# Performance work log

Measured on AMD Instinct MI355X. Metric: run time of the kernel, lower is better.

## Reference

```python
import jax, jax.numpy as jnp
import numpy as np
from jax import lax

# --- model constants (match init_kwargs) ---
B = 4096
T, N_FEAT = 100, 81
KH = 7                 # cnn_kernel_height
T_MOD = T - KH + 1     # 94
M = 100                # cnn_hidden_size
P = 128                # decoder hidden size
SKIP = 10
SH = 32                # skip_hidden_size
PT = T_MOD // SKIP     # 9


def setup_inputs() -> dict:
    key = jax.random.key(0)
    ks = jax.random.split(key, 18)
    s = 0.05
    def rn(k, shape, scale=s):
        return jax.random.normal(k, shape, dtype=jnp.float32) * scale
    return {
        "enc_data": jax.random.normal(ks[0], (B, T, N_FEAT), dtype=jnp.float32),
        # Conv2d(1 -> M, kernel=(KH, N_FEAT))
        "conv_w": rn(ks[1], (M, 1, KH, N_FEAT)),
        "conv_b": rn(ks[2], (M,)),
        # TemporalAttention: W_d: Linear(2P->M, no bias), U_d: Linear(M->M, no bias), v_d: Linear(M->1, no bias)
        "Wd": rn(ks[3], (M, 2 * P)),
        "Ud": rn(ks[4], (M, M)),
        "vd": rn(ks[5], (1, M)),
        # LSTM(input=M, hidden=P), PyTorch gate order i,f,g,o
        "lstm_wih": rn(ks[6], (4 * P, M)),
        "lstm_whh": rn(ks[7], (4 * P, P)),
        "lstm_bih": rn(ks[8], (4 * P,)),
        "lstm_bhh": rn(ks[9], (4 * P,)),
        # GRU(input=M, hidden=SH), PyTorch gate order r,z,n
        "gru_wih": rn(ks[10], (3 * SH, M)),
        "gru_whh": rn(ks[11], (3 * SH, SH)),
        "gru_bih": rn(ks[12], (3 * SH,)),
        "gru_bhh": rn(ks[13], (3 * SH,)),
        # output head: Linear(M+P+SKIP*SH -> P), ReLU, (Dropout=eval identity), Linear(P -> 1)
        "out1_w": rn(ks[14], (P, M + P + SKIP * SH)),
        "out1_b": rn(ks[15], (P,)),
        "out2_w": rn(ks[16], (1, P)),
        "out2_b": rn(ks[17], (1,)),
    }


def reference(enc_data, conv_w, conv_b, Wd, Ud, vd,
              lstm_wih, lstm_whh, lstm_bih, lstm_bhh,
              gru_wih, gru_whh, gru_bih, gru_bhh,
              out1_w, out1_b, out2_w, out2_b):
    b = enc_data.shape[0]

    # --- CNN encoder: Conv2d valid over full feature width -> [B, T_MOD, M] ---
    x = enc_data[:, None]  # [B,1,T,n]
    h = lax.conv_general_dilated(x, conv_w, window_strides=(1, 1), padding='VALID',
                                 dimension_numbers=('NCHW', 'OIHW', 'NCHW'))  # [B,M,T_MOD,1]
    H = jax.nn.relu(h + conv_b[None, :, None, None])[..., 0].transpose(0, 2, 1)  # [B,T_MOD,M]

    # precompute U_d(H) once (same math; U_d applied to H is step-invariant)
    HU = jnp.einsum('btm,km->btk', H, Ud)  # [B,T_MOD,M]

    def dec_step(carry, _):
        d, s = carry  # each [B,P]
        q = jnp.concatenate([d, s], axis=1)                       # [B,2P]
        e = jnp.tanh((q @ Wd.T)[:, None, :] + HU)                 # [B,T_MOD,M]
        scores = jnp.einsum('btm,m->bt', e, vd[0])                # [B,T_MOD]
        beta = jax.nn.softmax(scores, axis=1)                     # softmax over time
        c = jnp.einsum('bt,btm->bm', beta, H)                     # context [B,M]
        gates = c @ lstm_wih.T + lstm_bih + d @ lstm_whh.T + lstm_bhh
        i_g, f_g, g_g, o_g = jnp.split(gates, 4, axis=1)
        s_new = jax.nn.sigmoid(f_g) * s + jax.nn.sigmoid(i_g) * jnp.tanh(g_g)
        d_new = jax.nn.sigmoid(o_g) * jnp.tanh(s_new)
        return (d_new, s_new), (beta, c)

    d0 = jnp.zeros((b, P), dtype=enc_data.dtype)
    s0 = jnp.zeros((b, P), dtype=enc_data.dtype)
    (d_T, _), (betas, cs) = lax.scan(dec_step, (d0, s0), None, length=T_MOD)
    c_last = cs[-1]                                               # [B,M]
    dec_out = jnp.concatenate([d_T, c_last], axis=1)              # [B, P+M]

    # --- skip GRU over strided conv features ---
    Hs = H[:, -PT * SKIP:, :]                                     # [B, PT*SKIP, M]
    Hs = (Hs.transpose(0, 2, 1)                                   # [B, M, PT*SKIP]
            .reshape(b, M, PT, SKIP)
            .transpose(2, 0, 3, 1)                                # [PT, B, SKIP, M]
            .reshape(PT, b * SKIP, M))

    def gru_step(hprev, xt):
        gi = xt @ gru_wih.T + gru_bih
        gh = hprev @ gru_whh.T + gru_bhh
        ir, iz, inn = jnp.split(gi, 3, axis=1)
        hr, hz, hn = jnp.split(gh, 3, axis=1)
        r = jax.nn.sigmoid(ir + hr)
        z = jax.nn.sigmoid(iz + hz)
        nn_ = jnp.tanh(inn + r * hn)
        hnew = (1.0 - z) * nn_ + z * hprev
        return hnew, None

    h0 = jnp.zeros((b * SKIP, SH), dtype=enc_data.dtype)
    h_skip, _ = lax.scan(gru_step, h0, Hs)                        # [B*SKIP, SH]
    h_skip = h_skip.reshape(b, SKIP * SH)                         # matches torch view

    feat = jnp.concatenate([dec_out, h_skip], axis=1)             # [B, P+M+SKIP*SH]
    out = jax.nn.relu(feat @ out1_w.T + out1_b) @ out2_w.T + out2_b  # [B,1]
    return out[:, 0]
```

## Files before the change

kernel.cpp:

```cpp
#include <hip/hip_runtime.h>

typedef unsigned int u32;
typedef unsigned short u16;
typedef _Float16 half2_t __attribute__((ext_vector_type(2)));

#define TM 94
#define NB 2
#define DEC_NT 512

__device__ __forceinline__ float bf2f(u16 v){ return __builtin_bit_cast(float, ((u32)v)<<16); }
__device__ __forceinline__ float bflo(u32 v){ return __builtin_bit_cast(float, v<<16); }
__device__ __forceinline__ float bfhi(u32 v){ return __builtin_bit_cast(float, v & 0xffff0000u); }
__device__ __forceinline__ u32 f2bf_bits(float f){ u32 u=__builtin_bit_cast(u32,f); return (u + 0x7fffu + ((u>>16)&1u))>>16; }
__device__ __forceinline__ u32 packbf2(float a, float b){ return f2bf_bits(a) | (f2bf_bits(b)<<16); }
__device__ __forceinline__ u32 packh2(float a, float b){ half2_t h; h.x=(_Float16)a; h.y=(_Float16)b; return __builtin_bit_cast(u32,h); }
__device__ __forceinline__ float fdot2(u32 a, u32 b, float c){
  return __builtin_amdgcn_fdot2(__builtin_bit_cast(half2_t,a), __builtin_bit_cast(half2_t,b), c, false);
}
__device__ __forceinline__ float fast_rcp(float x){ return __builtin_amdgcn_rcpf(x); }
__device__ __forceinline__ float sigmoid_f(float x){ return fast_rcp(1.f + __expf(-x)); }
__device__ __forceinline__ float tanh_f(float x){ float e=__expf(2.f*x); return 1.f - 2.f*fast_rcp(e+1.f); }

__global__ __launch_bounds__(256)
void prep_kernel(const float* __restrict__ wih, const float* __restrict__ whh,
                 const float* __restrict__ Wd,
                 uint4* __restrict__ WgT, uint4* __restrict__ WdT2)
{
  int idx = blockIdx.x*256 + threadIdx.x;
  if (idx < 16384){
    int t = idx & 1023;
    int j = idx >> 10;
    int h = t >> 9, g = t & 511;
    u32 r[4];
    #pragma unroll
    for (int s=0;s<4;s++){
      int u = 4*j + s;
      u32 v = 0u;
      if (h==0){ if (u < 50) v = packh2(wih[g*100+2*u], wih[g*100+2*u+1]); }
      else     { if (u < 64) v = packh2(whh[g*128+2*u], whh[g*128+2*u+1]); }
      r[s]=v;
    }
    WgT[idx] = make_uint4(r[0],r[1],r[2],r[3]);
  } else {
    int idx2 = idx - 16384;
    int t = idx2 & 511;
    int i = idx2 >> 9;
    int mw = t >> 2, part = t & 3;
    u32 r[4] = {0u,0u,0u,0u};
    if (mw < 100){
      int ii = (i + 2*part) & 7;
      const float* wd = Wd + mw*256 + 2*(part*32 + ii*4);
      #pragma unroll
      for (int k=0;k<4;k++) r[k] = packh2(wd[2*k], wd[2*k+1]);
    }
    WdT2[idx2] = make_uint4(r[0],r[1],r[2],r[3]);
  }
}

__global__ __launch_bounds__(128)
void conv_kernel(const float* __restrict__ enc, const float* __restrict__ cw,
                 const float* __restrict__ cb, u16* __restrict__ Hb)
{
  __shared__ float sE[8100];
  const int tid = threadIdx.x;
  const int b = blockIdx.y;
  const int chunk = blockIdx.x;
  const float* ep = enc + (size_t)b*8100;
  for (int i=tid;i<8100;i+=128) sE[i]=ep[i];
  __syncthreads();
  if (tid >= TM) return;
  const int t = tid;
  const int mo = chunk*10;
  const float* wb = cw + mo*567;
  float acc[10];
  #pragma unroll
  for (int k=0;k<10;k++) acc[k]=cb[mo+k];
  const float* e = sE + t*81;
  #pragma unroll 3
  for (int j=0;j<567;j++){
    float ev = e[j];
    #pragma unroll
    for (int k=0;k<10;k++) acc[k] += ev*wb[k*567+j];
  }
  u32* out = (u32*)Hb + ((size_t)b*9400 + t*100 + mo)/2;
  #pragma unroll
  for (int k=0;k<5;k++) out[k] = packbf2(fmaxf(acc[2*k],0.f), fmaxf(acc[2*k+1],0.f));
}

#define OFF_SHU 37600
#define OFF_SQ  75200
#define OFF_SZ  76224
#define OFF_SVD 77248
#define OFF_AB  77648
#define DEC_LDS 79696

__global__ __launch_bounds__(DEC_NT) __attribute__((amdgpu_waves_per_eu(2, 4)))
void decoder_kernel(const u16* __restrict__ Hb, const float* __restrict__ Ud,
                    const float* __restrict__ vd,
                    const uint4* __restrict__ WgT, const uint4* __restrict__ WdT2,
                    const float* __restrict__ bih, const float* __restrict__ bhh,
                    float* __restrict__ dT, float* __restrict__ cLast)
{
  extern __shared__ char smem[];
  u16*      sH   = (u16*)smem;
  u16*      sHU  = (u16*)(smem + OFF_SHU);
  u32*      sq32 = (u32*)(smem + OFF_SQ);
  _Float16* sq16 = (_Float16*)(smem + OFF_SQ);
  u32*      sz32 = (u32*)(smem + OFF_SZ);
  _Float16* sz16 = (_Float16*)(smem + OFF_SZ);
  float*    svd  = (float*)(smem + OFF_SVD);
  float*    sa   = (float*)(smem + OFF_AB);
  float*    sbeta= (float*)(smem + OFF_AB + 800);
  _Float16* sg16 = (_Float16*)(smem + OFF_AB);

  const int tid = threadIdx.x;
  const int b0 = blockIdx.x * NB;

  {
    const uint4* src = (const uint4*)(Hb + (size_t)b0*9400);
    uint4* dst = (uint4*)sH;
    for (int i=tid;i<2350;i+=DEC_NT) dst[i]=src[i];
  }
  if (tid < 100) svd[tid] = vd[tid];
  for (int i=tid;i<NB*128;i+=DEC_NT){ sq32[i]=0u; sz32[i]=0u; }
  __syncthreads();

  for (int idx=tid; idx<4700; idx+=DEC_NT){
    int kq = idx/188;
    int r  = idx - kq*188;
    int bi = r/94;
    int t  = r - 94*bi;
    const u32* hrow = (const u32*)sH + bi*4700 + t*50;
    const float* ud0 = Ud + (kq*4+0)*100;
    const float* ud1 = Ud + (kq*4+1)*100;
    const float* ud2 = Ud + (kq*4+2)*100;
    const float* ud3 = Ud + (kq*4+3)*100;
    float c0=0.f,c1=0.f,c2=0.f,c3=0.f;
    #pragma unroll 5
    for (int mq=0; mq<25; mq++){
      uint2 hp = *(const uint2*)(hrow + mq*2);
      float h0=bflo(hp.x), h1=bfhi(hp.x), h2=bflo(hp.y), h3=bfhi(hp.y);
      float4 u0 = *(const float4*)(ud0 + mq*4);
      float4 u1 = *(const float4*)(ud1 + mq*4);
      float4 u2 = *(const float4*)(ud2 + mq*4);
      float4 u3 = *(const float4*)(ud3 + mq*4);
      c0 += h0*u0.x + h1*u0.y + h2*u0.z + h3*u0.w;
      c1 += h0*u1.x + h1*u1.y + h2*u1.z + h3*u1.w;
      c2 += h0*u2.x + h1*u2.y + h2*u2.z + h3*u2.w;
      c3 += h0*u3.x + h1*u3.y + h2*u3.z + h3*u3.w;
    }
    u32* dst = (u32*)sHU + bi*4700 + t*50 + kq*2;
    dst[0] = packbf2(c0,c1);
    dst[1] = packbf2(c2,c3);
  }
  __syncthreads();

  const int mw = tid>>2, part = tid&3;
  uint4 wv[8];
  if (mw < 100){
    #pragma unroll
    for (int i=0;i<8;i++) wv[i] = WdT2[i*512 + tid];
  }
  const float biasg = bih[tid] + bhh[tid];
  const uint4* wp0 = WgT + tid;
  const uint4* wp1 = WgT + 512 + tid;

  float s_reg = 0.f;

  #pragma unroll 1
  for (int step=0; step<TM; step++){
    if (mw < 100){
      #pragma unroll 1
      for (int bi=0;bi<NB;bi++){
        const u32* qb = sq32 + bi*128 + part*32;
        float a0=0.f, a1=0.f;
        #pragma unroll
        for (int i=0;i<8;i++){
          int ii = (i+2*part)&7;
          uint4 qv = *(const uint4*)(qb + ii*4);
          a0 = fdot2(wv[i].x, qv.x, a0);
          a1 = fdot2(wv[i].y, qv.y, a1);
          a0 = fdot2(wv[i].z, qv.z, a0);
          a1 = fdot2(wv[i].w, qv.w, a1);
        }
        float acc = a0+a1;
        acc += __shfl_xor(acc,1);
        acc += __shfl_xor(acc,2);
        if (part==0) sa[bi*100+mw]=acc;
      }
    }
    __syncthreads();
    if (tid < NB*188){
      int row = tid>>1, th = tid&1;
      int bi = row/94;
      int t  = row - 94*bi;
      const uint4* hu4 = (const uint4*)((const u32*)sHU + bi*4700 + t*50 + th*24);
      const float4* ap = (const float4*)(sa + bi*100) + th*12;
      const float4* vp = (const float4*)svd + th*12;
      float acc=0.f;
      #pragma unroll
      for (int c=0;c<6;c++){
        uint4 h4 = hu4[c];
        float4 a0 = ap[2*c], a1 = ap[2*c+1];
        float4 v0 = vp[2*c], v1 = vp[2*c+1];
        acc += v0.x*tanh_f(a0.x + bflo(h4.x));
        acc += v0.y*tanh_f(a0.y + bfhi(h4.x));
        acc += v0.z*tanh_f(a0.z + bflo(h4.y));
        acc += v0.w*tanh_f(a0.w + bfhi(h4.y));
        acc += v1.x*tanh_f(a1.x + bflo(h4.z));
        acc += v1.y*tanh_f(a1.y + bfhi(h4.z));
        acc += v1.z*tanh_f(a1.z + bflo(h4.w));
        acc += v1.w*tanh_f(a1.w + bfhi(h4.w));
      }
      if (th){
        uint2 ht = *(const uint2*)((const u32*)hu4 + 24);
        float4 a = ap[12]; float4 v = vp[12];
        acc += v.x*tanh_f(a.x + bflo(ht.x));
        acc += v.y*tanh_f(a.y + bfhi(ht.x));
        acc += v.z*tanh_f(a.z + bflo(ht.y));
        acc += v.w*tanh_f(a.w + bfhi(ht.y));
      }
      acc += __shfl_xor(acc,1);
      if (!th) sbeta[bi*96+t]=acc;
    }
    __syncthreads();
    if (tid < 64*NB){
      int bi = tid>>6, lane = tid&63;
      float s0 = sbeta[bi*96+lane];
      float s1 = (lane<30)? sbeta[bi*96+64+lane] : -1e30f;
      float mx = fmaxf(s0,s1);
      #pragma unroll
      for (int o=32;o>=1;o>>=1) mx = fmaxf(mx, __shfl_xor(mx,o));
      float e0 = __expf(s0-mx);
      float e1 = (lane<30)? __expf(s1-mx) : 0.f;
      float sm = e0+e1;
      #pragma unroll
      for (int o=32;o>=1;o>>=1) sm += __shfl_xor(sm,o);
      float rs = fast_rcp(sm);
      sbeta[bi*96+lane] = e0*rs;
      if (lane<30) sbeta[bi*96+64+lane] = e1*rs;
    }
    __syncthreads();
    if (tid < NB*200){
      int bi = tid/200;
      int r  = tid - 200*bi;
      int mp = r>>2, th = r&3;
      int tstart = (th<2) ? th*24 : 48+(th-2)*23;
      const float* bp = sbeta + bi*96 + tstart;
      const u32* hp = (const u32*)sH + bi*4700 + tstart*50 + mp;
      float a0=0.f, a1=0.f;
      #pragma unroll
      for (int i=0;i<23;i++){
        float be = bp[i];
        u32 h = hp[i*50];
        a0 += be*bflo(h); a1 += be*bfhi(h);
      }
      if (th<2){
        float be = bp[23]; u32 h = hp[23*50];
        a0 += be*bflo(h); a1 += be*bfhi(h);
      }
      a0 += __shfl_xor(a0,1); a1 += __shfl_xor(a1,1);
      a0 += __shfl_xor(a0,2); a1 += __shfl_xor(a1,2);
      if (th==0){
        sz32[bi*128+mp] = packh2(a0,a1);
        if (step==TM-1){
          cLast[(size_t)(b0+bi)*100 + 2*mp]   = a0;
          cLast[(size_t)(b0+bi)*100 + 2*mp+1] = a1;
        }
      }
    }
    __syncthreads();
    {
      float acc0 = biasg, acc1 = biasg;
      const u32* zc0 = sz32;
      const u32* zc1 = sz32 + 128;
      #pragma unroll 1
      for (int jb=0; jb<16; jb+=4){
        uint4 w[4], v[4];
        #pragma unroll
        for (int k=0;k<4;k++) w[k] = wp0[(jb+k)*1024];
        #pragma unroll
        for (int k=0;k<4;k++) v[k] = wp1[(jb+k)*1024];
        #pragma unroll
        for (int k=0;k<4;k++){
          int j = jb+k;
          uint4 zA0 = *(const uint4*)(zc0 + 4*j);
          uint4 zA1 = *(const uint4*)(zc1 + 4*j);
          acc0 = fdot2(w[k].x, zA0.x, acc0); acc0 = fdot2(w[k].y, zA0.y, acc0);
          acc0 = fdot2(w[k].z, zA0.z, acc0); acc0 = fdot2(w[k].w, zA0.w, acc0);
          acc1 = fdot2(w[k].x, zA1.x, acc1); acc1 = fdot2(w[k].y, zA1.y, acc1);
          acc1 = fdot2(w[k].z, zA1.z, acc1); acc1 = fdot2(w[k].w, zA1.w, acc1);
          uint4 zB0 = *(const uint4*)(zc0 + 64 + 4*j);
          uint4 zB1 = *(const uint4*)(zc1 + 64 + 4*j);
          acc0 = fdot2(v[k].x, zB0.x, acc0); acc0 = fdot2(v[k].y, zB0.y, acc0);
          acc0 = fdot2(v[k].z, zB0.z, acc0); acc0 = fdot2(v[k].w, zB0.w, acc0);
          acc1 = fdot2(v[k].x, zB1.x, acc1); acc1 = fdot2(v[k].y, zB1.y, acc1);
          acc1 = fdot2(v[k].z, zB1.z, acc1); acc1 = fdot2(v[k].w, zB1.w, acc1);
        }
      }
      sg16[      tid] = (_Float16)acc0;
      sg16[512 + tid] = (_Float16)acc1;
    }
    __syncthreads();
    if (tid < 128*NB){
      int bi = tid>>7, p = tid&127;
      float ig = (float)sg16[bi*512+p];
      float fg = (float)sg16[bi*512+128+p];
      float gg_= (float)sg16[bi*512+256+p];
      float og = (float)sg16[bi*512+384+p];
      float sn = sigmoid_f(fg)*s_reg + sigmoid_f(ig)*tanh_f(gg_);
      float dn = sigmoid_f(og)*tanh_f(sn);
      s_reg = sn;
      sq16[bi*256+p]      = (_Float16)dn;
      sq16[bi*256+128+p]  = (_Float16)sn;
      sz16[bi*256+128+p]  = (_Float16)dn;
      if (step==TM-1) dT[(size_t)(b0+bi)*128+p]=dn;
    }
    __syncthreads();
  }
}

__global__ __launch_bounds__(256)
void gru_kernel(const u16* __restrict__ Hb, const float* __restrict__ wih,
                const float* __restrict__ whh, const float* __restrict__ bihp,
                const float* __restrict__ bhhp, float* __restrict__ hskip)
{
  __shared__ float sWih[96][101];
  __shared__ float sWhh[96][33];
  __shared__ float sxt[8][100];
  __shared__ float sh[8][33];
  const int tid = threadIdx.x;
  for (int i=tid;i<9600;i+=256){ sWih[i/100][i%100]=wih[i]; }
  for (int i=tid;i<3072;i+=256){ sWhh[i>>5][i&31]=whh[i]; }
  const int r = tid>>5, j = tid&31;
  const int rowg = blockIdx.x*8 + r;
  const int b = rowg/10, sk = rowg - b*10;
  const float b_r = bihp[j], b_z = bihp[32+j], b_n = bihp[64+j];
  const float hb_r = bhhp[j], hb_z = bhhp[32+j], hb_n = bhhp[64+j];
  sh[r][j]=0.f;
  float h = 0.f;
  __syncthreads();
  for (int pt=0; pt<9; pt++){
    for (int i=tid;i<800;i+=256){
      int rr=i/100, m=i-rr*100;
      int rg = blockIdx.x*8+rr; int bb=rg/10, ss=rg-bb*10;
      sxt[rr][m] = bf2f(Hb[(size_t)bb*9400 + (size_t)(4+pt*10+ss)*100 + m]);
    }
    __syncthreads();
    float gi_r=b_r, gi_z=b_z, gi_n=b_n, gh_r=hb_r, gh_z=hb_z, gh_n=hb_n;
    #pragma unroll 4
    for (int m=0;m<100;m++){
      float x = sxt[r][m];
      gi_r += sWih[j][m]*x; gi_z += sWih[32+j][m]*x; gi_n += sWih[64+j][m]*x;
    }
    #pragma unroll
    for (int k=0;k<32;k++){
      float hp = sh[r][k];
      gh_r += sWhh[j][k]*hp; gh_z += sWhh[32+j][k]*hp; gh_n += sWhh[64+j][k]*hp;
    }
    float rg_ = sigmoid_f(gi_r+gh_r);
    float z  = sigmoid_f(gi_z+gh_z);
    float n  = tanh_f(gi_n + rg_*gh_n);
    h = (1.f-z)*n + z*h;
    __syncthreads();
    sh[r][j]=h;
    __syncthreads();
  }
  hskip[(size_t)b*320 + sk*32 + j] = h;
}

#define OUT_NB 32
#define OUT_LDS ((OUT_NB*552 + 8*552)*4)

__global__ __launch_bounds__(256)
void out_kernel(const float* __restrict__ dT, const float* __restrict__ cLast,
                const float* __restrict__ hskip, const float* __restrict__ w1,
                const float* __restrict__ b1, const float* __restrict__ w2,
                const float* __restrict__ b2, float* __restrict__ outp)
{
  extern __shared__ float osm[];
  float* sf = osm;
  float* sw = osm + OUT_NB*552;
  const int tid = threadIdx.x;
  const int b0 = blockIdx.x*OUT_NB;
  for (int i=tid;i<OUT_NB*548;i+=256){
    int bl = i/548, k = i - 548*bl; int b = b0+bl;
    float v;
    if (k<128) v = dT[(size_t)b*128+k];
    else if (k<228) v = cLast[(size_t)b*100+(k-128)];
    else v = hskip[(size_t)b*320+(k-228)];
    sf[bl*552+k]=v;
  }
  const int bl = tid>>3, j = tid&7;
  float outv = 0.f;
  for (int jt=0; jt<128; jt+=8){
    __syncthreads();
    for (int i=tid;i<8*548;i+=256){
      int rr=i/548, c=i-548*rr;
      sw[rr*552+c] = w1[(size_t)jt*548 + i];
    }
    __syncthreads();
    float acc = b1[jt+j];
    const float* fr = sf + bl*552;
    const float* wr = sw + j*552;
    #pragma unroll 4
    for (int k=0;k<548;k++) acc += fr[k]*wr[k];
    outv += fmaxf(acc,0.f)*w2[jt+j];
  }
  outv += __shfl_xor(outv,1);
  outv += __shfl_xor(outv,2);
  outv += __shfl_xor(outv,4);
  if (j==0) outp[b0+bl] = outv + b2[0];
}

extern "C" void kernel_launch(void* const* d_in, const int* in_sizes, int n_in,
                              void* d_out, int out_size, void* d_ws, size_t ws_size,
                              hipStream_t stream)
{
  const float* enc      = (const float*)d_in[0];
  const float* conv_w   = (const float*)d_in[1];
  const float* conv_b   = (const float*)d_in[2];
  const float* Wd       = (const float*)d_in[3];
  const float* Ud       = (const float*)d_in[4];
  const float* vd       = (const float*)d_in[5];
  const float* lstm_wih = (const float*)d_in[6];
  const float* lstm_whh = (const float*)d_in[7];
  const float* lstm_bih = (const float*)d_in[8];
  const float* lstm_bhh = (const float*)d_in[9];
  const float* gru_wih  = (const float*)d_in[10];
  const float* gru_whh  = (const float*)d_in[11];
  const float* gru_bih  = (const float*)d_in[12];
  const float* gru_bhh  = (const float*)d_in[13];
  const float* out1_w   = (const float*)d_in[14];
  const float* out1_b   = (const float*)d_in[15];
  const float* out2_w   = (const float*)d_in[16];
  const float* out2_b   = (const float*)d_in[17];

  char* ws = (char*)d_ws;
  u16*   Hb    = (u16*)ws;
  float* dT    = (float*)(ws + 77004800);
  float* cLast = (float*)(ws + 79101952);
  float* hskip = (float*)(ws + 80740352);
  uint4* WgT   = (uint4*)(ws + 80740352);
  uint4* WdT2  = (uint4*)(ws + 81002496);

  prep_kernel<<<80, 256, 0, stream>>>(lstm_wih, lstm_whh, Wd, WgT, WdT2);

  conv_kernel<<<dim3(10,4096,1), 128, 0, stream>>>(enc, conv_w, conv_b, Hb);

  (void)hipFuncSetAttribute((const void*)decoder_kernel,
                            hipFuncAttributeMaxDynamicSharedMemorySize, DEC_LDS);
  decoder_kernel<<<4096/NB, DEC_NT, DEC_LDS, stream>>>(Hb, Ud, vd, WgT, WdT2,
                                                       lstm_bih, lstm_bhh,
                                                       dT, cLast);

  gru_kernel<<<5120, 256, 0, stream>>>(Hb, gru_wih, gru_whh, gru_bih, gru_bhh, hskip);

  (void)hipFuncSetAttribute((const void*)out_kernel,
                            hipFuncAttributeMaxDynamicSharedMemorySize, OUT_LDS);
  out_kernel<<<4096/OUT_NB, 256, OUT_LDS, stream>>>(dT, cLast, hskip, out1_w, out1_b,
                                                    out2_w, out2_b, (float*)d_out);
}
```

Measured before the change: 7.351 ms.

## Move attention U_d projection to global scratch and halve decoder LDS footprint

The decoder kernel now keeps the precomputed H·U_d projection in a per-block global scratch buffer (padded rows) instead of LDS. The d/s/z vectors are packed into one compact shared region, with the weight layout in prep_kernel reordered to match, so the attention and gate dot products skip the zero-padded words. LDS per block drops to about half, which should let more blocks sit on each CU. The grid is fixed at 1024 persistent blocks that each process two batch pairs in sequence. The cost is per-step global/L2 reads of the projection instead of LDS reads, and fewer blocks in the grid.

Result: slower. 8.167 ms (+11.1%).

```diff
diff --git a/kernel.cpp b/kernel.cpp
--- a/kernel.cpp
+++ b/kernel.cpp
@@ -7,6 +7,7 @@
 #define TM 94
 #define NB 2
 #define DEC_NT 512
+#define DEC_GRID 1024
 
 __device__ __forceinline__ float bf2f(u16 v){ return __builtin_bit_cast(float, ((u32)v)<<16); }
 __device__ __forceinline__ float bflo(u32 v){ return __builtin_bit_cast(float, v<<16); }
@@ -24,7 +25,7 @@
 __global__ __launch_bounds__(256)
 void prep_kernel(const float* __restrict__ wih, const float* __restrict__ whh,
                  const float* __restrict__ Wd,
-                 uint4* __restrict__ WgT, uint4* __restrict__ WdT2)
+                 uint4* __restrict__ WgT, uint4* __restrict__ WdT3)
 {
   int idx = blockIdx.x*256 + threadIdx.x;
   if (idx < 16384){
@@ -48,12 +49,12 @@
     int mw = t >> 2, part = t & 3;
     u32 r[4] = {0u,0u,0u,0u};
     if (mw < 100){
-      int ii = (i + 2*part) & 7;
-      const float* wd = Wd + mw*256 + 2*(part*32 + ii*4);
+      int bu = (i<4) ? (part*16 + 4*i) : (64 + part*16 + 4*(i-4));
+      const float* wd = Wd + mw*256 + 2*bu;
       #pragma unroll
       for (int k=0;k<4;k++) r[k] = packh2(wd[2*k], wd[2*k+1]);
     }
-    WdT2[idx2] = make_uint4(r[0],r[1],r[2],r[3]);
+    WdT3[idx2] = make_uint4(r[0],r[1],r[2],r[3]);
   }
 }
 
@@ -87,236 +88,257 @@
   for (int k=0;k<5;k++) out[k] = packbf2(fmaxf(acc[2*k],0.f), fmaxf(acc[2*k+1],0.f));
 }
 
-#define OFF_SHU 37600
-#define OFF_SQ  75200
-#define OFF_SZ  76224
-#define OFF_SVD 77248
-#define OFF_AB  77648
-#define DEC_LDS 79696
+#define OFF_SZQ   37600
+#define OFF_STAIL 38624
+#define OFF_UNI   38752
+#define DEC_LDS   40800
 
 __global__ __launch_bounds__(DEC_NT) __attribute__((amdgpu_waves_per_eu(2, 4)))
 void decoder_kernel(const u16* __restrict__ Hb, const float* __restrict__ Ud,
                     const float* __restrict__ vd,
-                    const uint4* __restrict__ WgT, const uint4* __restrict__ WdT2,
+                    const uint4* __restrict__ WgT, const uint4* __restrict__ WdT3,
                     const float* __restrict__ bih, const float* __restrict__ bhh,
-                    float* __restrict__ dT, float* __restrict__ cLast)
+                    u32* __restrict__ HUscr, float* __restrict__ dT,
+                    float* __restrict__ cLast)
 {
   extern __shared__ char smem[];
   u16*      sH   = (u16*)smem;
-  u16*      sHU  = (u16*)(smem + OFF_SHU);
-  u32*      sq32 = (u32*)(smem + OFF_SQ);
-  _Float16* sq16 = (_Float16*)(smem + OFF_SQ);
-  u32*      sz32 = (u32*)(smem + OFF_SZ);
-  _Float16* sz16 = (_Float16*)(smem + OFF_SZ);
-  float*    svd  = (float*)(smem + OFF_SVD);
-  float*    sa   = (float*)(smem + OFF_AB);
-  float*    sbeta= (float*)(smem + OFF_AB + 800);
-  _Float16* sg16 = (_Float16*)(smem + OFF_AB);
+  float*    sa   = (float*)(smem + OFF_UNI);
+  float*    sbeta= (float*)(smem + OFF_UNI + 800);
+  _Float16* sg16 = (_Float16*)(smem + OFF_UNI);
 
   const int tid = threadIdx.x;
-  const int b0 = blockIdx.x * NB;
-
-  {
-    const uint4* src = (const uint4*)(Hb + (size_t)b0*9400);
-    uint4* dst = (uint4*)sH;
-    for (int i=tid;i<2350;i+=DEC_NT) dst[i]=src[i];
-  }
-  if (tid < 100) svd[tid] = vd[tid];
-  for (int i=tid;i<NB*128;i+=DEC_NT){ sq32[i]=0u; sz32[i]=0u; }
-  __syncthreads();
-
-  for (int idx=tid; idx<4700; idx+=DEC_NT){
-    int kq = idx/188;
-    int r  = idx - kq*188;
-    int bi = r/94;
-    int t  = r - 94*bi;
-    const u32* hrow = (const u32*)sH + bi*4700 + t*50;
-    const float* ud0 = Ud + (kq*4+0)*100;
-    const float* ud1 = Ud + (kq*4+1)*100;
-    const float* ud2 = Ud + (kq*4+2)*100;
-    const float* ud3 = Ud + (kq*4+3)*100;
-    float c0=0.f,c1=0.f,c2=0.f,c3=0.f;
-    #pragma unroll 5
-    for (int mq=0; mq<25; mq++){
-      uint2 hp = *(const uint2*)(hrow + mq*2);
-      float h0=bflo(hp.x), h1=bfhi(hp.x), h2=bflo(hp.y), h3=bfhi(hp.y);
-      float4 u0 = *(const float4*)(ud0 + mq*4);
-      float4 u1 = *(const float4*)(ud1 + mq*4);
-      float4 u2 = *(const float4*)(ud2 + mq*4);
-      float4 u3 = *(const float4*)(ud3 + mq*4);
-      c0 += h0*u0.x + h1*u0.y + h2*u0.z + h3*u0.w;
-      c1 += h0*u1.x + h1*u1.y + h2*u1.z + h3*u1.w;
-      c2 += h0*u2.x + h1*u2.y + h2*u2.z + h3*u2.w;
-      c3 += h0*u3.x + h1*u3.y + h2*u3.z + h3*u3.w;
-    }
-    u32* dst = (u32*)sHU + bi*4700 + t*50 + kq*2;
-    dst[0] = packbf2(c0,c1);
-    dst[1] = packbf2(c2,c3);
-  }
-  __syncthreads();
-
   const int mw = tid>>2, part = tid&3;
+
   uint4 wv[8];
   if (mw < 100){
     #pragma unroll
-    for (int i=0;i<8;i++) wv[i] = WdT2[i*512 + tid];
+    for (int i=0;i<8;i++) wv[i] = WdT3[i*512 + tid];
   }
   const float biasg = bih[tid] + bhh[tid];
   const uint4* wp0 = WgT + tid;
   const uint4* wp1 = WgT + 512 + tid;
-
-  float s_reg = 0.f;
+  u32* hub = HUscr + (size_t)blockIdx.x * 9776;
 
   #pragma unroll 1
-  for (int step=0; step<TM; step++){
-    if (mw < 100){
-      #pragma unroll 1
-      for (int bi=0;bi<NB;bi++){
-        const u32* qb = sq32 + bi*128 + part*32;
+  for (int pr=0; pr<2; ++pr){
+    const int pair = blockIdx.x + pr*DEC_GRID;
+    const int b0 = pair*NB;
+
+    {
+      const uint4* src = (const uint4*)(Hb + (size_t)b0*9400);
+      uint4* dst = (uint4*)sH;
+      for (int i=tid;i<2350;i+=DEC_NT) dst[i]=src[i];
+      for (int i=tid;i<288;i+=DEC_NT) ((u32*)(smem+OFF_SZQ))[i]=0u;
+    }
+    __syncthreads();
+    for (int idx=tid; idx<4700; idx+=DEC_NT){
+      int kq = idx/188;
+      int r  = idx - kq*188;
+      int bi = r/94;
+      int t  = r - 94*bi;
+      const u32* hrow = (const u32*)sH + bi*4700 + t*50;
+      const float* ud0 = Ud + (kq*4+0)*100;
+      const float* ud1 = Ud + (kq*4+1)*100;
+      const float* ud2 = Ud + (kq*4+2)*100;
+      const float* ud3 = Ud + (kq*4+3)*100;
+      float c0=0.f,c1=0.f,c2=0.f,c3=0.f;
+      #pragma unroll 5
+      for (int mq=0; mq<25; mq++){
+        uint2 hp = *(const uint2*)(hrow + mq*2);
+        float h0=bflo(hp.x), h1=bfhi(hp.x), h2=bflo(hp.y), h3=bfhi(hp.y);
+        float4 u0 = *(const float4*)(ud0 + mq*4);
+        float4 u1 = *(const float4*)(ud1 + mq*4);
+        float4 u2 = *(const float4*)(ud2 + mq*4);
+        float4 u3 = *(const float4*)(ud3 + mq*4);
+        c0 += h0*u0.x + h1*u0.y + h2*u0.z + h3*u0.w;
+        c1 += h0*u1.x + h1*u1.y + h2*u1.z + h3*u1.w;
+        c2 += h0*u2.x + h1*u2.y + h2*u2.z + h3*u2.w;
+        c3 += h0*u3.x + h1*u3.y + h2*u3.z + h3*u3.w;
+      }
+      u32* dst = hub + bi*4888 + t*52 + kq*2;
+      dst[0] = packbf2(c0,c1);
+      dst[1] = packbf2(c2,c3);
+    }
+    float s_reg = 0.f;
+    __syncthreads();
+
+    #pragma unroll 1
+    for (int step=0; step<TM; step++){
+      if (mw < 100){
+        #pragma unroll 1
+        for (int bi=0;bi<NB;bi++){
+          const char* zb = smem + OFF_SZQ + bi*512;
+          const uint4* qd = (const uint4*)(zb + 208) + part*4;
+          const uint4* qs = (part<3) ? ((const uint4*)zb + part*4)
+                                     : (const uint4*)(smem + OFF_STAIL + bi*64);
+          float a0=0.f, a1=0.f;
+          #pragma unroll
+          for (int i=0;i<4;i++){
+            uint4 qv = qd[i];
+            a0 = fdot2(wv[i].x, qv.x, a0);
+            a1 = fdot2(wv[i].y, qv.y, a1);
+            a0 = fdot2(wv[i].z, qv.z, a0);
+            a1 = fdot2(wv[i].w, qv.w, a1);
+          }
+          #pragma unroll
+          for (int i=0;i<4;i++){
+            uint4 qv = qs[i];
+            a0 = fdot2(wv[4+i].x, qv.x, a0);
+            a1 = fdot2(wv[4+i].y, qv.y, a1);
+            a0 = fdot2(wv[4+i].z, qv.z, a0);
+            a1 = fdot2(wv[4+i].w, qv.w, a1);
+          }
+          float acc = a0+a1;
+          acc += __shfl_xor(acc,1);
+          acc += __shfl_xor(acc,2);
+          if (part==0) sa[bi*100+mw]=acc;
+        }
+      }
+      __syncthreads();
+      if (tid < 376){
+        int row = tid>>1, th = tid&1;
+        int bi = row/94;
+        int t  = row - 94*bi;
+        const uint4* hu4 = (const uint4*)(hub + bi*4888 + t*52) + th*6;
+        const float4* ap = (const float4*)(sa + bi*100) + th*12;
+        const float4* vp = (const float4*)vd + th*12;
+        float acc=0.f;
+        #pragma unroll
+        for (int c=0;c<6;c++){
+          uint4 h4 = hu4[c];
+          float4 a0 = ap[2*c], a1 = ap[2*c+1];
+          float4 v0 = vp[2*c], v1 = vp[2*c+1];
+          acc += v0.x*tanh_f(a0.x + bflo(h4.x));
+          acc += v0.y*tanh_f(a0.y + bfhi(h4.x));
+          acc += v0.z*tanh_f(a0.z + bflo(h4.y));
+          acc += v0.w*tanh_f(a0.w + bfhi(h4.y));
+          acc += v1.x*tanh_f(a1.x + bflo(h4.z));
+          acc += v1.y*tanh_f(a1.y + bfhi(h4.z));
+          acc += v1.z*tanh_f(a1.z + bflo(h4.w));
+          acc += v1.w*tanh_f(a1.w + bfhi(h4.w));
+        }
+        if (th){
+          uint2 ht = *(const uint2*)((const u32*)hu4 + 24);
+          float4 a = ap[12]; float4 v = vp[12];
+          acc += v.x*tanh_f(a.x + bflo(ht.x));
+          acc += v.y*tanh_f(a.y + bfhi(ht.x));
+          acc += v.z*tanh_f(a.z + bflo(ht.y));
+          acc += v.w*tanh_f(a.w + bfhi(ht.y));
+        }
+        acc += __shfl_xor(acc,1);
+        if (!th) sbeta[bi*96+t]=acc;
+      }
+      __syncthreads();
+      if (tid < 64*NB){
+        int bi = tid>>6, lane = tid&63;
+        float s0 = sbeta[bi*96+lane];
+        float s1 = (lane<30)? sbeta[bi*96+64+lane] : -1e30f;
+        float mx = fmaxf(s0,s1);
+        #pragma unroll
+        for (int o=32;o>=1;o>>=1) mx = fmaxf(mx, __shfl_xor(mx,o));
+        float e0 = __expf(s0-mx);
+        float e1 = (lane<30)? __expf(s1-mx) : 0.f;
+        float sm = e0+e1;
+        #pragma unroll
+        for (int o=32;o>=1;o>>=1) sm += __shfl_xor(sm,o);
+        float rs = fast_rcp(sm);
+        sbeta[bi*96+lane] = e0*rs;
+        if (lane<30) sbeta[bi*96+64+lane] = e1*rs;
+      }
+      __syncthreads();
+      if (tid < NB*200){
+        int bi = tid/200;
+        int r  = tid - 200*bi;
+        int mp = r>>2, th = r&3;
+        int tstart = (th<2) ? th*24 : 48+(th-2)*23;
+        const float* bp = sbeta + bi*96 + tstart;
+        const u32* hp = (const u32*)sH + bi*4700 + tstart*50 + mp;
         float a0=0.f, a1=0.f;
         #pragma unroll
-        for (int i=0;i<8;i++){
-          int ii = (i+2*part)&7;
-          uint4 qv = *(const uint4*)(qb + ii*4);
-          a0 = fdot2(wv[i].x, qv.x, a0);
-          a1 = fdot2(wv[i].y, qv.y, a1);
-          a0 = fdot2(wv[i].z, qv.z, a0);
-          a1 = fdot2(wv[i].w, qv.w, a1);
-        }
-        float acc = a0+a1;
-        acc += __shfl_xor(acc,1);
-        acc += __shfl_xor(acc,2);
-        if (part==0) sa[bi*100+mw]=acc;
-      }
-    }
-    __syncthreads();
-    if (tid < NB*188){
-      int row = tid>>1, th = tid&1;
-      int bi = row/94;
-      int t  = row - 94*bi;
-      const uint4* hu4 = (const uint4*)((const u32*)sHU + bi*4700 + t*50 + th*24);
-      const float4* ap = (const float4*)(sa + bi*100) + th*12;
-      const float4* vp = (const float4*)svd + th*12;
-      float acc=0.f;
-      #pragma unroll
-      for (int c=0;c<6;c++){
-        uint4 h4 = hu4[c];
-        float4 a0 = ap[2*c], a1 = ap[2*c+1];
-        float4 v0 = vp[2*c], v1 = vp[2*c+1];
-        acc += v0.x*tanh_f(a0.x + bflo(h4.x));
-        acc += v0.y*tanh_f(a0.y + bfhi(h4.x));
-        acc += v0.z*tanh_f(a0.z + bflo(h4.y));
-        acc += v0.w*tanh_f(a0.w + bfhi(h4.y));
-        acc += v1.x*tanh_f(a1.x + bflo(h4.z));
-        acc += v1.y*tanh_f(a1.y + bfhi(h4.z));
-        acc += v1.z*tanh_f(a1.z + bflo(h4.w));
-        acc += v1.w*tanh_f(a1.w + bfhi(h4.w));
-      }
-      if (th){
-        uint2 ht = *(const uint2*)((const u32*)hu4 + 24);
-        float4 a = ap[12]; float4 v = vp[12];
-        acc += v.x*tanh_f(a.x + bflo(ht.x));
-        acc += v.y*tanh_f(a.y + bfhi(ht.x));
-        acc += v.z*tanh_f(a.z + bflo(ht.y));
-        acc += v.w*tanh_f(a.w + bfhi(ht.y));
-      }
-      acc += __shfl_xor(acc,1);
-      if (!th) sbeta[bi*96+t]=acc;
-    }
-    __syncthreads();
-    if (tid < 64*NB){
-      int bi = tid>>6, lane = tid&63;
-      float s0 = sbeta[bi*96+lane];
-      float s1 = (lane<30)? sbeta[bi*96+64+lane] : -1e30f;
-      float mx = fmaxf(s0,s1);
-      #pragma unroll
-      for (int o=32;o>=1;o>>=1) mx = fmaxf(mx, __shfl_xor(mx,o));
-      float e0 = __expf(s0-mx);
-      float e1 = (lane<30)? __expf(s1-mx) : 0.f;
-      float sm = e0+e1;
-      #pragma unroll
-      for (int o=32;o>=1;o>>=1) sm += __shfl_xor(sm,o);
-      float rs = fast_rcp(sm);
-      sbeta[bi*96+lane] = e0*rs;
-      if (lane<30) sbeta[bi*96+64+lane] = e1*rs;
-    }
-    __syncthreads();
-    if (tid < NB*200){
-      int bi = tid/200;
-      int r  = tid - 200*bi;
-      int mp = r>>2, th = r&3;
-      int tstart = (th<2) ? th*24 : 48+(th-2)*23;
-      const float* bp = sbeta + bi*96 + tstart;
-      const u32* hp = (const u32*)sH + bi*4700 + tstart*50 + mp;
-      float a0=0.f, a1=0.f;
-      #pragma unroll
-      for (int i=0;i<23;i++){
-        float be = bp[i];
-        u32 h = hp[i*50];
-        a0 += be*bflo(h); a1 += be*bfhi(h);
-      }
-      if (th<2){
-        float be = bp[23]; u32 h = hp[23*50];
-        a0 += be*bflo(h); a1 += be*bfhi(h);
-      }
-      a0 += __shfl_xor(a0,1); a1 += __shfl_xor(a1,1);
-      a0 += __shfl_xor(a0,2); a1 += __shfl_xor(a1,2);
-      if (th==0){
-        sz32[bi*128+mp] = packh2(a0,a1);
-        if (step==TM-1){
-          cLast[(size_t)(b0+bi)*100 + 2*mp]   = a0;
-          cLast[(size_t)(b0+bi)*100 + 2*mp+1] = a1;
-        }
-      }
-    }
-    __syncthreads();
-    {
-      float acc0 = biasg, acc1 = biasg;
-      const u32* zc0 = sz32;
-      const u32* zc1 = sz32 + 128;
-      #pragma unroll 1
-      for (int jb=0; jb<16; jb+=4){
-        uint4 w[4], v[4];
-        #pragma unroll
-        for (int k=0;k<4;k++) w[k] = wp0[(jb+k)*1024];
-        #pragma unroll
-        for (int k=0;k<4;k++) v[k] = wp1[(jb+k)*1024];
-        #pragma unroll
-        for (int k=0;k<4;k++){
-          int j = jb+k;
-          uint4 zA0 = *(const uint4*)(zc0 + 4*j);
-          uint4 zA1 = *(const uint4*)(zc1 + 4*j);
-          acc0 = fdot2(w[k].x, zA0.x, acc0); acc0 = fdot2(w[k].y, zA0.y, acc0);
-          acc0 = fdot2(w[k].z, zA0.z, acc0); acc0 = fdot2(w[k].w, zA0.w, acc0);
-          acc1 = fdot2(w[k].x, zA1.x, acc1); acc1 = fdot2(w[k].y, zA1.y, acc1);
-          acc1 = fdot2(w[k].z, zA1.z, acc1); acc1 = fdot2(w[k].w, zA1.w, acc1);
-          uint4 zB0 = *(const uint4*)(zc0 + 64 + 4*j);
-          uint4 zB1 = *(const uint4*)(zc1 + 64 + 4*j);
-          acc0 = fdot2(v[k].x, zB0.x, acc0); acc0 = fdot2(v[k].y, zB0.y, acc0);
-          acc0 = fdot2(v[k].z, zB0.z, acc0); acc0 = fdot2(v[k].w, zB0.w, acc0);
-          acc1 = fdot2(v[k].x, zB1.x, acc1); acc1 = fdot2(v[k].y, zB1.y, acc1);
-          acc1 = fdot2(v[k].z, zB1.z, acc1); acc1 = fdot2(v[k].w, zB1.w, acc1);
-        }
-      }
-      sg16[      tid] = (_Float16)acc0;
-      sg16[512 + tid] = (_Float16)acc1;
-    }
-    __syncthreads();
-    if (tid < 128*NB){
-      int bi = tid>>7, p = tid&127;
-      float ig = (float)sg16[bi*512+p];
-      float fg = (float)sg16[bi*512+128+p];
-      float gg_= (float)sg16[bi*512+256+p];
-      float og = (float)sg16[bi*512+384+p];
-      float sn = sigmoid_f(fg)*s_reg + sigmoid_f(ig)*tanh_f(gg_);
-      float dn = sigmoid_f(og)*tanh_f(sn);
-      s_reg = sn;
-      sq16[bi*256+p]      = (_Float16)dn;
-      sq16[bi*256+128+p]  = (_Float16)sn;
-      sz16[bi*256+128+p]  = (_Float16)dn;
-      if (step==TM-1) dT[(size_t)(b0+bi)*128+p]=dn;
-    }
-    __syncthreads();
+        for (int i=0;i<23;i++){
+          float be = bp[i];
+          u32 h = hp[i*50];
+          a0 += be*bflo(h); a1 += be*bfhi(h);
+        }
+        if (th<2){
+          float be = bp[23]; u32 h = hp[23*50];
+          a0 += be*bflo(h); a1 += be*bfhi(h);
+        }
+        a0 += __shfl_xor(a0,1); a1 += __shfl_xor(a1,1);
+        a0 += __shfl_xor(a0,2); a1 += __shfl_xor(a1,2);
+        if (th==0){
+          ((u32*)(smem + OFF_SZQ + bi*512))[mp] = packh2(a0,a1);
+          if (step==TM-1){
+            cLast[(size_t)(b0+bi)*100 + 2*mp]   = a0;
+            cLast[(size_t)(b0+bi)*100 + 2*mp+1] = a1;
+          }
+        }
+      }
+      __syncthreads();
+      {
+        float acc0 = biasg, acc1 = biasg;
+        const u32* c0 = (const u32*)(smem + OFF_SZQ);
+        const u32* c1 = (const u32*)(smem + OFF_SZQ + 512);
+        const u32* d0 = (const u32*)(smem + OFF_SZQ + 208);
+        const u32* d1 = (const u32*)(smem + OFF_SZQ + 512 + 208);
+        #pragma unroll 1
+        for (int jb=0; jb<12; jb+=4){
+          uint4 w[4];
+          #pragma unroll
+          for (int k=0;k<4;k++) w[k] = wp0[(jb+k)*1024];
+          #pragma unroll
+          for (int k=0;k<4;k++){
+            int j = jb+k;
+            uint4 z0 = *(const uint4*)(c0 + 4*j);
+            uint4 z1 = *(const uint4*)(c1 + 4*j);
+            acc0 = fdot2(w[k].x, z0.x, acc0); acc0 = fdot2(w[k].y, z0.y, acc0);
+            acc0 = fdot2(w[k].z, z0.z, acc0); acc0 = fdot2(w[k].w, z0.w, acc0);
+            acc1 = fdot2(w[k].x, z1.x, acc1); acc1 = fdot2(w[k].y, z1.y, acc1);
+            acc1 = fdot2(w[k].z, z1.z, acc1); acc1 = fdot2(w[k].w, z1.w, acc1);
+          }
+        }
+        {
+          uint4 we = wp0[12*1024];
+          acc0 = fdot2(we.x, c0[48], acc0); acc0 = fdot2(we.y, c0[49], acc0);
+          acc1 = fdot2(we.x, c1[48], acc1); acc1 = fdot2(we.y, c1[49], acc1);
+        }
+        #pragma unroll 1
+        for (int jb=0; jb<16; jb+=4){
+          uint4 v[4];
+          #pragma unroll
+          for (int k=0;k<4;k++) v[k] = wp1[(jb+k)*1024];
+          #pragma unroll
+          for (int k=0;k<4;k++){
+            int j = jb+k;
+            uint4 z0 = *(const uint4*)(d0 + 4*j);
+            uint4 z1 = *(const uint4*)(d1 + 4*j);
+            acc0 = fdot2(v[k].x, z0.x, acc0); acc0 = fdot2(v[k].y, z0.y, acc0);
+            acc0 = fdot2(v[k].z, z0.z, acc0); acc0 = fdot2(v[k].w, z0.w, acc0);
+            acc1 = fdot2(v[k].x, z1.x, acc1); acc1 = fdot2(v[k].y, z1.y, acc1);
+            acc1 = fdot2(v[k].z, z1.z, acc1); acc1 = fdot2(v[k].w, z1.w, acc1);
+          }
+        }
+        sg16[      tid] = (_Float16)acc0;
+        sg16[512 + tid] = (_Float16)acc1;
+      }
+      __syncthreads();
+      if (tid < 128*NB){
+        int bi = tid>>7, p = tid&127;
+        float ig = (float)sg16[bi*512+p];
+        float fg = (float)sg16[bi*512+128+p];
+        float gg_= (float)sg16[bi*512+256+p];
+        float og = (float)sg16[bi*512+384+p];
+        float sn = sigmoid_f(fg)*s_reg + sigmoid_f(ig)*tanh_f(gg_);
+        float dn = sigmoid_f(og)*tanh_f(sn);
+        s_reg = sn;
+        ((_Float16*)(smem + OFF_SZQ + bi*512 + 208))[p] = (_Float16)dn;
+        if (p < 96) ((_Float16*)(smem + OFF_SZQ + bi*512))[p] = (_Float16)sn;
+        else        ((_Float16*)(smem + OFF_STAIL + bi*64))[p-96] = (_Float16)sn;
+        if (step==TM-1) dT[(size_t)(b0+bi)*128+p]=dn;
+      }
+      __syncthreads();
+    }
   }
 }
 
@@ -442,17 +464,18 @@
   float* cLast = (float*)(ws + 79101952);
   float* hskip = (float*)(ws + 80740352);
   uint4* WgT   = (uint4*)(ws + 80740352);
-  uint4* WdT2  = (uint4*)(ws + 81002496);
-
-  prep_kernel<<<80, 256, 0, stream>>>(lstm_wih, lstm_whh, Wd, WgT, WdT2);
+  uint4* WdT3  = (uint4*)(ws + 81002496);
+  u32*   HUscr = (u32*)(ws + 85983232);
+
+  prep_kernel<<<80, 256, 0, stream>>>(lstm_wih, lstm_whh, Wd, WgT, WdT3);
 
   conv_kernel<<<dim3(10,4096,1), 128, 0, stream>>>(enc, conv_w, conv_b, Hb);
 
   (void)hipFuncSetAttribute((const void*)decoder_kernel,
                             hipFuncAttributeMaxDynamicSharedMemorySize, DEC_LDS);
-  decoder_kernel<<<4096/NB, DEC_NT, DEC_LDS, stream>>>(Hb, Ud, vd, WgT, WdT2,
-                                                       lstm_bih, lstm_bhh,
-                                                       dT, cLast);
+  decoder_kernel<<<DEC_GRID, DEC_NT, DEC_LDS, stream>>>(Hb, Ud, vd, WgT, WdT3,
+                                                        lstm_bih, lstm_bhh,
+                                                        HUscr, dT, cLast);
 
   gru_kernel<<<5120, 256, 0, stream>>>(Hb, gru_wih, gru_whh, gru_bih, gru_bhh, hskip);
 
```
